# Kernel optimization log

Hardware: AMD Instinct MI355X
Metric: run time of the kernel (lower is better)

Reference implementation:

```python
import jax, jax.numpy as jnp
import numpy as np

B, S, E = 2, 2048, 2048
NQ, NKV, HD = 16, 4, 128
WINDOW = 512
ROPE_BASE = 10000.0


def _rope(x):
    # x: [B, H, S, HD], interleaved even/odd rotation
    half = HD // 2
    freqs = 1.0 / (ROPE_BASE ** (2.0 * jnp.arange(half, dtype=jnp.float32) / HD))
    pos = jnp.arange(x.shape[2], dtype=jnp.float32)
    ang = pos[:, None] * freqs[None, :]            # [S, HD/2]
    cos = jnp.cos(ang)[None, None].astype(x.dtype)  # [1,1,S,HD/2]
    sin = jnp.sin(ang)[None, None].astype(x.dtype)
    xe = x[..., 0::2]
    xo = x[..., 1::2]
    re = xe * cos - xo * sin
    ro = xe * sin + xo * cos
    return jnp.stack([re, ro], axis=-1).reshape(x.shape)


def setup_inputs() -> dict:
    key = jax.random.key(0)
    ks = jax.random.split(key, 9)
    s_in = 1.0 / np.sqrt(E)
    s_out = 1.0 / np.sqrt(NQ * HD)
    return {
        "x": jax.random.normal(ks[0], (B, S, E), jnp.float32),
        "Wq": jax.random.normal(ks[1], (E, NQ * HD), jnp.float32) * s_in,
        "bq": jax.random.normal(ks[2], (NQ * HD,), jnp.float32) * 0.01,
        "Wk": jax.random.normal(ks[3], (E, NKV * HD), jnp.float32) * s_in,
        "bk": jax.random.normal(ks[4], (NKV * HD,), jnp.float32) * 0.01,
        "Wv": jax.random.normal(ks[5], (E, NKV * HD), jnp.float32) * s_in,
        "bv": jax.random.normal(ks[6], (NKV * HD,), jnp.float32) * 0.01,
        "Wo": jax.random.normal(ks[7], (NQ * HD, E), jnp.float32) * s_out,
        "bo": jax.random.normal(ks[8], (E,), jnp.float32) * 0.01,
    }


def reference(x, Wq, bq, Wk, bk, Wv, bv, Wo, bo):
    b, s, _ = x.shape
    q = (x @ Wq + bq).reshape(b, s, NQ, HD).transpose(0, 2, 1, 3)   # [B,NQ,S,HD]
    k = (x @ Wk + bk).reshape(b, s, NKV, HD).transpose(0, 2, 1, 3)  # [B,NKV,S,HD]
    v = (x @ Wv + bv).reshape(b, s, NKV, HD).transpose(0, 2, 1, 3)
    q = _rope(q)
    k = _rope(k)
    rep = NQ // NKV
    k = jnp.repeat(k, rep, axis=1)  # [B,NQ,S,HD], matches torch repeat pattern
    v = jnp.repeat(v, rep, axis=1)
    scores = jnp.einsum("bhqd,bhkd->bhqk", q, k) / np.sqrt(HD)
    i = jnp.arange(s)[:, None]
    j = jnp.arange(s)[None, :]
    allowed = (j <= i) & ((i - j) <= WINDOW)  # sliding-window causal mask
    scores = jnp.where(allowed[None, None], scores, -jnp.inf)
    weights = jax.nn.softmax(scores, axis=-1)
    out = jnp.einsum("bhqk,bhkd->bhqd", weights, v)
    out = out.transpose(0, 2, 1, 3).reshape(b, s, NQ * HD)
    return out @ Wo + bo
```

## Files before the change

### kernel.cpp

```cpp
#include <hip/hip_runtime.h>
#include <hip/hip_bf16.h>
#include <math.h>

#define BB 2
#define SS 2048
#define EE 2048
#define NQ 16
#define NKV 4
#define HD 128
#define WINDOW 512

typedef __hip_bfloat16 bf16;
typedef short short8 __attribute__((ext_vector_type(8)));
typedef float f32x4 __attribute__((ext_vector_type(4)));

__device__ __forceinline__ float toF(bf16 v) { return __bfloat162float(v); }
__device__ __forceinline__ bf16 toB(float v) { return __float2bfloat16(v); }

__device__ __forceinline__ void gld_lds16(const void* g, void* l) {
    __builtin_amdgcn_global_load_lds(
        (const __attribute__((address_space(1))) void*)g,
        (__attribute__((address_space(3))) void*)l, 16, 0, 0);
}

__global__ __launch_bounds__(256) void convert_bf16(const float* __restrict__ in,
                                                    bf16* __restrict__ out, int n) {
    int i = (blockIdx.x * 256 + threadIdx.x) * 4;
    if (i >= n) return;
    const float4 v = *(const float4*)(in + i);
    bf16 o[4] = {toB(v.x), toB(v.y), toB(v.z), toB(v.w)};
    *(uint2*)(out + i) = *(const uint2*)o;
}

__global__ __launch_bounds__(256) void convert_transpose(const float* __restrict__ in,
                                                         bf16* __restrict__ out,
                                                         int K, int N) {
    __shared__ float tile[32][33];
    const int t = threadIdx.x;
    const int tx = t & 31, ty = t >> 5;
    const int n0 = blockIdx.x * 32, k0 = blockIdx.y * 32;
#pragma unroll
    for (int r = 0; r < 4; r++)
        tile[ty + r * 8][tx] = in[(size_t)(k0 + ty + r * 8) * N + n0 + tx];
    __syncthreads();
#pragma unroll
    for (int r = 0; r < 4; r++)
        out[(size_t)(n0 + ty + r * 8) * K + k0 + tx] = toB(tile[tx][ty + r * 8]);
}

__global__ __launch_bounds__(256) void convert_transpose_qkv(
    const float* __restrict__ Wq, const float* __restrict__ Wk,
    const float* __restrict__ Wv, bf16* __restrict__ out) {
    __shared__ float tile[32][33];
    const int t = threadIdx.x;
    const int tx = t & 31, ty = t >> 5;
    const int n0 = blockIdx.x * 32, k0 = blockIdx.y * 32;
    const float* src; int N, nl0;
    if (n0 < 2048)      { src = Wq; N = 2048; nl0 = n0; }
    else if (n0 < 2560) { src = Wk; N = 512;  nl0 = n0 - 2048; }
    else                { src = Wv; N = 512;  nl0 = n0 - 2560; }
#pragma unroll
    for (int r = 0; r < 4; r++)
        tile[ty + r * 8][tx] = src[(size_t)(k0 + ty + r * 8) * N + nl0 + tx];
    __syncthreads();
#pragma unroll
    for (int r = 0; r < 4; r++)
        out[(size_t)(n0 + ty + r * 8) * 2048 + k0 + tx] = toB(tile[tx][ty + r * 8]);
}

template <int MODE>
__global__ __launch_bounds__(256) void mfma_gemm(
    const bf16* __restrict__ A, const bf16* __restrict__ BT,
    const float* __restrict__ b0, const float* __restrict__ b1,
    const float* __restrict__ b2,
    float* __restrict__ Yf,
    bf16* __restrict__ Yq, bf16* __restrict__ Yk, bf16* __restrict__ Yv,
    int M, int N, int K) {
    __shared__ bf16 As[128 * 32];
    __shared__ bf16 Bs[128 * 32];

    const int t = threadIdx.x;
    const int lane = t & 63;
    const int w = t >> 6;
    const int wm = w >> 1, wn = w & 1;
    const int m0 = blockIdx.y * 128, n0 = blockIdx.x * 128;

    const int srow = lane >> 2;
    const int sg   = lane & 3;
    const int scol = (sg ^ ((srow >> 1) & 3)) * 8;

    f32x4 acc[4][4];
#pragma unroll
    for (int i = 0; i < 4; i++)
#pragma unroll
        for (int j = 0; j < 4; j++) acc[i][j] = (f32x4)0.f;

    const int lr = lane & 15;
    const int lq = lane >> 4;
    const int slotr = (lq ^ ((lr >> 1) & 3)) * 8;

    for (int k0 = 0; k0 < K; k0 += 32) {
#pragma unroll
        for (int s = 0; s < 2; s++) {
            const int c = w * 2 + s;
            gld_lds16(A + (size_t)(m0 + c * 16 + srow) * K + k0 + scol, As + c * 512);
            gld_lds16(BT + (size_t)(n0 + c * 16 + srow) * K + k0 + scol, Bs + c * 512);
        }
        __syncthreads();
        short8 af[4], bfv[4];
#pragma unroll
        for (int i = 0; i < 4; i++)
            af[i] = *(const short8*)(As + (wm * 64 + i * 16 + lr) * 32 + slotr);
#pragma unroll
        for (int j = 0; j < 4; j++)
            bfv[j] = *(const short8*)(Bs + (wn * 64 + j * 16 + lr) * 32 + slotr);
#pragma unroll
        for (int i = 0; i < 4; i++)
#pragma unroll
            for (int j = 0; j < 4; j++)
                acc[i][j] = __builtin_amdgcn_mfma_f32_16x16x32_bf16(af[i], bfv[j],
                                                                    acc[i][j], 0, 0, 0);
        __syncthreads();
    }

    if (MODE == 0) {
#pragma unroll
        for (int j = 0; j < 4; j++) {
            const int col = n0 + wn * 64 + j * 16 + lr;
            const float bj = b0[col];
#pragma unroll
            for (int i = 0; i < 4; i++) {
                const int row = m0 + wm * 64 + i * 16 + lq * 4;
#pragma unroll
                for (int r = 0; r < 4; r++)
                    Yf[(size_t)(row + r) * N + col] = acc[i][j][r] + bj;
            }
        }
    } else if (n0 < 2560) {
        bf16* outp; const float* bias; int ldc, c0;
        if (n0 < 2048) { outp = Yq; bias = b0; ldc = 2048; c0 = n0; }
        else           { outp = Yk; bias = b1; ldc = 512;  c0 = n0 - 2048; }
#pragma unroll
        for (int j = 0; j < 4; j++) {
            const int col = c0 + wn * 64 + j * 16 + lr;
            const float bj = bias[col];
            const int d2 = (col & 127) >> 1;
            const bool odd = col & 1;
            const float freq = __expf(-0.14384103622589045f * (float)d2);
#pragma unroll
            for (int i = 0; i < 4; i++) {
                const int row = m0 + wm * 64 + i * 16 + lq * 4;
#pragma unroll
                for (int r = 0; r < 4; r++) {
                    const float v = acc[i][j][r] + bj;
                    const float p = __shfl_xor(v, 1, 64);
                    const float ang = (float)((row + r) & (SS - 1)) * freq;
                    float sn, cs;
                    __sincosf(ang, &sn, &cs);
                    const float o = odd ? (p * sn + v * cs) : (v * cs - p * sn);
                    outp[(size_t)(row + r) * ldc + col] = toB(o);
                }
            }
        }
    } else {
        const int c0 = n0 - 2560;
#pragma unroll
        for (int j = 0; j < 4; j++) {
            const int col = c0 + wn * 64 + j * 16 + lr;
            const float bj = b2[col];
            const int hkv = col >> 7, d = col & 127;
#pragma unroll
            for (int i = 0; i < 4; i++) {
                const int row = m0 + wm * 64 + i * 16 + lq * 4;
                const int bb = row >> 11, sr = row & (SS - 1);
                union { bf16 b[4]; uint2 u; } o4;
#pragma unroll
                for (int r = 0; r < 4; r++) o4.b[r] = toB(acc[i][j][r] + bj);
                *(uint2*)(Yv + (((size_t)bb * NKV + hkv) * HD + d) * SS + sr) = o4.u;
            }
        }
    }
}

__global__ __launch_bounds__(256) void attn_mfma(const bf16* __restrict__ Q,
                                                 const bf16* __restrict__ K,
                                                 const bf16* __restrict__ VT,
                                                 bf16* __restrict__ Oout) {
    __shared__ bf16 Ks[64 * 128];
    __shared__ bf16 Vs[128 * 64];
    __shared__ bf16 Ps[4 * 16 * 72];

    const int t = threadIdx.x;
    const int lane = t & 63;
    const int w = t >> 6;
    const int q0 = blockIdx.x * 64;
    const int h = blockIdx.y;
    const int b = blockIdx.z;
    const int hkv = h >> 2;
    const int lr = lane & 15;
    const int lq = lane >> 4;
    const float scale = 0.08838834764831845f;

    short8 aq[4];
    {
        const int q = q0 + w * 16 + lr;
        const bf16* qp = Q + (((size_t)b * SS + q) * NQ + h) * HD + lq * 8;
#pragma unroll
        for (int ks = 0; ks < 4; ks++) aq[ks] = *(const short8*)(qp + ks * 32);
    }

    const int krow = w * 16 + (lane >> 4);
    const int vrow = w * 32 + (lane >> 3);
    const bf16* Kbase = K + ((size_t)b * SS * NKV + hkv) * HD;
    const bf16* Vbase = VT + (((size_t)b * NKV + hkv) * HD) * SS;

    f32x4 Oa[8];
#pragma unroll
    for (int nb = 0; nb < 8; nb++) Oa[nb] = (f32x4)0.f;
    float mprev[4] = {-3.0e38f, -3.0e38f, -3.0e38f, -3.0e38f};
    float lsum[4] = {0.f, 0.f, 0.f, 0.f};

    bf16* Pw = Ps + w * 16 * 72;
    const int jstart = (q0 >= WINDOW) ? (q0 - WINDOW) : 0;

    for (int c0 = jstart; c0 <= q0; c0 += 64) {
        __syncthreads();
#pragma unroll
        for (int s = 0; s < 4; s++) {
            const int r_ = krow + s * 4;
            const int g_ = (lane & 15) ^ (r_ & 7);
            gld_lds16(Kbase + (size_t)(c0 + r_) * (NKV * HD) + g_ * 8,
                      Ks + (w * 16 + s * 4) * 128);
        }
#pragma unroll
        for (int s = 0; s < 4; s++) {
            const int d_ = vrow + s * 8;
            const int g_ = (lane & 7) ^ (d_ & 7);
            gld_lds16(Vbase + (size_t)d_ * SS + c0 + g_ * 8,
                      Vs + (w * 32 + s * 8) * 64);
        }
        __syncthreads();

        f32x4 sa[4];
#pragma unroll
        for (int nb = 0; nb < 4; nb++) sa[nb] = (f32x4)0.f;
#pragma unroll
        for (int ks = 0; ks < 4; ks++) {
#pragma unroll
            for (int nb = 0; nb < 4; nb++) {
                const int slot = (ks * 4 + lq) ^ (lr & 7);
                short8 bk = *(const short8*)(Ks + (nb * 16 + lr) * 128 + slot * 8);
                sa[nb] = __builtin_amdgcn_mfma_f32_16x16x32_bf16(aq[ks], bk, sa[nb], 0, 0, 0);
            }
        }

        const int rowb = q0 + w * 16 + lq * 4;
        const bool noMask = (c0 + 63 <= q0 + w * 16) &&
                            (q0 + w * 16 + 15 - c0 <= WINDOW);
        float pr[4][4], alpha[4];
#pragma unroll
        for (int r = 0; r < 4; r++) {
            const int row = rowb + r;
            float sv[4];
            float mx = -3.0e38f;
            if (noMask) {
#pragma unroll
                for (int nb = 0; nb < 4; nb++) {
                    const float s = sa[nb][r] * scale;
                    sv[nb] = s;
                    mx = fmaxf(mx, s);
                }
            } else {
#pragma unroll
                for (int nb = 0; nb < 4; nb++) {
                    const int col = c0 + nb * 16 + lr;
                    const bool valid = (col <= row) && (row - col <= WINDOW);
                    const float s = valid ? sa[nb][r] * scale : -3.0e38f;
                    sv[nb] = s;
                    mx = fmaxf(mx, s);
                }
            }
#pragma unroll
            for (int off = 1; off < 16; off <<= 1) mx = fmaxf(mx, __shfl_xor(mx, off, 64));
            const float mn = fmaxf(fmaxf(mprev[r], mx), -1.0e30f);
            alpha[r] = __expf(mprev[r] - mn);
            mprev[r] = mn;
            float rs = 0.f;
#pragma unroll
            for (int nb = 0; nb < 4; nb++) {
                const float p = __expf(sv[nb] - mn);
                pr[r][nb] = p;
                rs += p;
            }
#pragma unroll
            for (int off = 1; off < 16; off <<= 1) rs += __shfl_xor(rs, off, 64);
            lsum[r] = lsum[r] * alpha[r] + rs;
        }

#pragma unroll
        for (int r = 0; r < 4; r++)
#pragma unroll
            for (int nb = 0; nb < 4; nb++)
                Pw[(lq * 4 + r) * 72 + nb * 16 + lr] = toB(pr[r][nb]);

#pragma unroll
        for (int nb = 0; nb < 8; nb++)
#pragma unroll
            for (int r = 0; r < 4; r++) Oa[nb][r] *= alpha[r];
#pragma unroll
        for (int ks = 0; ks < 2; ks++) {
            short8 pa = *(const short8*)(Pw + lr * 72 + ks * 32 + lq * 8);
#pragma unroll
            for (int nb = 0; nb < 8; nb++) {
                const int slot = (ks * 4 + lq) ^ (lr & 7);
                short8 bv = *(const short8*)(Vs + (nb * 16 + lr) * 64 + slot * 8);
                Oa[nb] = __builtin_amdgcn_mfma_f32_16x16x32_bf16(pa, bv, Oa[nb], 0, 0, 0);
            }
        }
    }

    float linv[4];
#pragma unroll
    for (int r = 0; r < 4; r++) linv[r] = 1.f / lsum[r];
    const int rowb = q0 + w * 16 + lq * 4;
#pragma unroll
    for (int nb = 0; nb < 8; nb++)
#pragma unroll
        for (int r = 0; r < 4; r++)
            Oout[(((size_t)b * SS + rowb + r) * NQ + h) * HD + nb * 16 + lr] =
                toB(Oa[nb][r] * linv[r]);
}

extern "C" void kernel_launch(void* const* d_in, const int* in_sizes, int n_in,
                              void* d_out, int out_size, void* d_ws, size_t ws_size,
                              hipStream_t stream) {
    const float* x  = (const float*)d_in[0];
    const float* Wq = (const float*)d_in[1];
    const float* bq = (const float*)d_in[2];
    const float* Wk = (const float*)d_in[3];
    const float* bk = (const float*)d_in[4];
    const float* Wv = (const float*)d_in[5];
    const float* bv = (const float*)d_in[6];
    const float* Wo = (const float*)d_in[7];
    const float* bo = (const float*)d_in[8];
    float* out = (float*)d_out;

    const int M   = BB * SS;
    const int DQ  = NQ * HD;
    const int DKV = NKV * HD;
    const int NPK = DQ + 2 * DKV;

    bf16* xb     = (bf16*)d_ws;
    bf16* WqkvT  = xb + (size_t)M * EE;
    bf16* WoT    = WqkvT + (size_t)NPK * EE;
    bf16* Qb     = WoT + (size_t)EE * DQ;
    bf16* Kb     = Qb + (size_t)M * DQ;
    bf16* Vb     = Kb + (size_t)M * DKV;

    convert_bf16<<<(M * EE / 4 + 255) / 256, 256, 0, stream>>>(x, xb, M * EE);
    convert_transpose_qkv<<<dim3(NPK / 32, EE / 32), 256, 0, stream>>>(Wq, Wk, Wv, WqkvT);
    convert_transpose<<<dim3(DQ / 32, DQ / 32), 256, 0, stream>>>(Wo, WoT, DQ, EE);

    mfma_gemm<1><<<dim3(NPK / 128, M / 128), 256, 0, stream>>>(
        xb, WqkvT, bq, bk, bv, nullptr, Qb, Kb, Vb, M, NPK, EE);

    attn_mfma<<<dim3(SS / 64, NQ, BB), 256, 0, stream>>>(Qb, Kb, Vb, Qb);

    mfma_gemm<0><<<dim3(EE / 128, M / 128), 256, 0, stream>>>(
        Qb, WoT, bo, nullptr, nullptr, out, nullptr, nullptr, nullptr, M, EE, DQ);
}
```

Measured before the change: 333.0 us.

## Use 256x256 double-buffered MFMA GEMM tiles with 512-thread blocks

Replaces the 128x128, K=32 single-buffered GEMM with a 256x256 tile over K=64 steps, run by 8 waves per block. Shared-memory staging is double-buffered: the next K tile is prefetched with global-to-LDS loads while MFMAs run on the current one. It also adds an XOR swizzle for 64-wide rows and raises wave priority around the MFMA bursts. The aim is more data reuse per loaded byte and less exposed load latency. The trade-off is far fewer blocks (192 and 128) than the GPU has CUs, plus 128KB of LDS per block, so only one block fits per CU.

```diff
diff --git a/kernel.cpp b/kernel.cpp
--- a/kernel.cpp
+++ b/kernel.cpp
@@ -69,58 +69,110 @@
 }
 
 template <int MODE>
-__global__ __launch_bounds__(256) void mfma_gemm(
+__global__ __launch_bounds__(512, 2) void mfma_gemm256(
     const bf16* __restrict__ A, const bf16* __restrict__ BT,
     const float* __restrict__ b0, const float* __restrict__ b1,
     const float* __restrict__ b2,
     float* __restrict__ Yf,
     bf16* __restrict__ Yq, bf16* __restrict__ Yk, bf16* __restrict__ Yv,
     int M, int N, int K) {
-    __shared__ bf16 As[128 * 32];
-    __shared__ bf16 Bs[128 * 32];
+    __shared__ __align__(16) bf16 As[2][2][128 * 64];
+    __shared__ __align__(16) bf16 Bs[2][2][128 * 64];
 
     const int t = threadIdx.x;
     const int lane = t & 63;
     const int w = t >> 6;
-    const int wm = w >> 1, wn = w & 1;
-    const int m0 = blockIdx.y * 128, n0 = blockIdx.x * 128;
-
-    const int srow = lane >> 2;
-    const int sg   = lane & 3;
-    const int scol = (sg ^ ((srow >> 1) & 3)) * 8;
-
-    f32x4 acc[4][4];
-#pragma unroll
-    for (int i = 0; i < 4; i++)
-#pragma unroll
-        for (int j = 0; j < 4; j++) acc[i][j] = (f32x4)0.f;
-
+    const int wm = w >> 2;
+    const int wn = w & 3;
+    const int m0 = blockIdx.y * 256, n0 = blockIdx.x * 256;
     const int lr = lane & 15;
     const int lq = lane >> 4;
-    const int slotr = (lq ^ ((lr >> 1) & 3)) * 8;
-
-    for (int k0 = 0; k0 < K; k0 += 32) {
-#pragma unroll
-        for (int s = 0; s < 2; s++) {
-            const int c = w * 2 + s;
-            gld_lds16(A + (size_t)(m0 + c * 16 + srow) * K + k0 + scol, As + c * 512);
-            gld_lds16(BT + (size_t)(n0 + c * 16 + srow) * K + k0 + scol, Bs + c * 512);
-        }
-        __syncthreads();
-        short8 af[4], bfv[4];
-#pragma unroll
-        for (int i = 0; i < 4; i++)
-            af[i] = *(const short8*)(As + (wm * 64 + i * 16 + lr) * 32 + slotr);
-#pragma unroll
-        for (int j = 0; j < 4; j++)
-            bfv[j] = *(const short8*)(Bs + (wn * 64 + j * 16 + lr) * 32 + slotr);
-#pragma unroll
-        for (int i = 0; i < 4; i++)
-#pragma unroll
-            for (int j = 0; j < 4; j++)
-                acc[i][j] = __builtin_amdgcn_mfma_f32_16x16x32_bf16(af[i], bfv[j],
-                                                                    acc[i][j], 0, 0, 0);
-        __syncthreads();
+
+    const int srow8 = lane >> 3;
+    const int sslot = lane & 7;
+    const int NT = K >> 6;
+
+    auto stA = [&](int bi, int h, int kt) {
+#pragma unroll
+        for (int l = 0; l < 2; l++) {
+            const int c = w * 2 + l;
+            const int r = c * 8 + srow8;
+            const int g = sslot ^ (r & 7);
+            gld_lds16(A + (size_t)(m0 + h * 128 + r) * K + kt * 64 + g * 8,
+                      &As[bi][h][c * 512]);
+        }
+    };
+    auto stB = [&](int bi, int h, int kt) {
+#pragma unroll
+        for (int l = 0; l < 2; l++) {
+            const int c = w * 2 + l;
+            const int r = c * 8 + srow8;
+            const int g = sslot ^ (r & 7);
+            gld_lds16(BT + (size_t)(n0 + h * 128 + r) * K + kt * 64 + g * 8,
+                      &Bs[bi][h][c * 512]);
+        }
+    };
+
+    f32x4 acc[8][4];
+#pragma unroll
+    for (int i = 0; i < 8; i++)
+#pragma unroll
+        for (int j = 0; j < 4; j++) acc[i][j] = (f32x4)0.f;
+
+    stA(0, 0, 0); stA(0, 1, 0); stB(0, 0, 0); stB(0, 1, 0);
+    asm volatile("s_waitcnt vmcnt(0)" ::: "memory");
+    __builtin_amdgcn_s_barrier();
+
+    const int brh0 = (wn & 1) * 64;
+    const int bh = wn >> 1;
+
+    for (int kt = 0; kt < NT; kt++) {
+        const int bi = kt & 1;
+        const bool pf = (kt + 1 < NT);
+        const bf16* Aw = &As[bi][wm][0];
+        const bf16* Bw = &Bs[bi][bh][0];
+        short8 bfr[4][2];
+#pragma unroll
+        for (int p = 0; p < 4; p++) {
+            if (p == 0 && pf) { stA(bi ^ 1, 0, kt + 1); stA(bi ^ 1, 1, kt + 1); }
+            if (p == 1 && pf) { stB(bi ^ 1, 0, kt + 1); stB(bi ^ 1, 1, kt + 1); }
+            if (p == 0) {
+#pragma unroll
+                for (int j = 0; j < 4; j++)
+#pragma unroll
+                    for (int kk = 0; kk < 2; kk++) {
+                        const int rh = brh0 + j * 16 + lr;
+                        const int slot = ((kk << 2) + lq) ^ (lr & 7);
+                        bfr[j][kk] = *(const short8*)(Bw + rh * 64 + slot * 8);
+                    }
+            }
+            short8 afr[2][2];
+#pragma unroll
+            for (int i2 = 0; i2 < 2; i2++)
+#pragma unroll
+                for (int kk = 0; kk < 2; kk++) {
+                    const int rh = (p * 2 + i2) * 16 + lr;
+                    const int slot = ((kk << 2) + lq) ^ (lr & 7);
+                    afr[i2][kk] = *(const short8*)(Aw + rh * 64 + slot * 8);
+                }
+            __builtin_amdgcn_s_barrier();
+            __builtin_amdgcn_s_setprio(1);
+#pragma unroll
+            for (int i2 = 0; i2 < 2; i2++)
+#pragma unroll
+                for (int j = 0; j < 4; j++)
+#pragma unroll
+                    for (int kk = 0; kk < 2; kk++)
+                        acc[p * 2 + i2][j] = __builtin_amdgcn_mfma_f32_16x16x32_bf16(
+                            afr[i2][kk], bfr[j][kk], acc[p * 2 + i2][j], 0, 0, 0);
+            __builtin_amdgcn_s_setprio(0);
+            if (p < 3) {
+                __builtin_amdgcn_s_barrier();
+            } else {
+                asm volatile("s_waitcnt vmcnt(0)" ::: "memory");
+                __builtin_amdgcn_s_barrier();
+            }
+        }
     }
 
     if (MODE == 0) {
@@ -129,8 +181,8 @@
             const int col = n0 + wn * 64 + j * 16 + lr;
             const float bj = b0[col];
 #pragma unroll
-            for (int i = 0; i < 4; i++) {
-                const int row = m0 + wm * 64 + i * 16 + lq * 4;
+            for (int i = 0; i < 8; i++) {
+                const int row = m0 + wm * 128 + i * 16 + lq * 4;
 #pragma unroll
                 for (int r = 0; r < 4; r++)
                     Yf[(size_t)(row + r) * N + col] = acc[i][j][r] + bj;
@@ -148,8 +200,8 @@
             const bool odd = col & 1;
             const float freq = __expf(-0.14384103622589045f * (float)d2);
 #pragma unroll
-            for (int i = 0; i < 4; i++) {
-                const int row = m0 + wm * 64 + i * 16 + lq * 4;
+            for (int i = 0; i < 8; i++) {
+                const int row = m0 + wm * 128 + i * 16 + lq * 4;
 #pragma unroll
                 for (int r = 0; r < 4; r++) {
                     const float v = acc[i][j][r] + bj;
@@ -170,8 +222,8 @@
             const float bj = b2[col];
             const int hkv = col >> 7, d = col & 127;
 #pragma unroll
-            for (int i = 0; i < 4; i++) {
-                const int row = m0 + wm * 64 + i * 16 + lq * 4;
+            for (int i = 0; i < 8; i++) {
+                const int row = m0 + wm * 128 + i * 16 + lq * 4;
                 const int bb = row >> 11, sr = row & (SS - 1);
                 union { bf16 b[4]; uint2 u; } o4;
 #pragma unroll
@@ -361,11 +413,11 @@
     convert_transpose_qkv<<<dim3(NPK / 32, EE / 32), 256, 0, stream>>>(Wq, Wk, Wv, WqkvT);
     convert_transpose<<<dim3(DQ / 32, DQ / 32), 256, 0, stream>>>(Wo, WoT, DQ, EE);
 
-    mfma_gemm<1><<<dim3(NPK / 128, M / 128), 256, 0, stream>>>(
+    mfma_gemm256<1><<<dim3(NPK / 256, M / 256), 512, 0, stream>>>(
         xb, WqkvT, bq, bk, bv, nullptr, Qb, Kb, Vb, M, NPK, EE);
 
     attn_mfma<<<dim3(SS / 64, NQ, BB), 256, 0, stream>>>(Qb, Kb, Vb, Qb);
 
-    mfma_gemm<0><<<dim3(EE / 128, M / 128), 256, 0, stream>>>(
+    mfma_gemm256<0><<<dim3(EE / 256, M / 256), 512, 0, stream>>>(
         Qb, WoT, bo, nullptr, nullptr, out, nullptr, nullptr, nullptr, M, EE, DQ);
 }
```

New measurement: 360.8 us. 8.4% more time.

## Rewrite projection GEMMs with larger tiles, 512 threads and double-buffered LDS prefetch

Applied to the files above, without the earlier changes.

Replaces the 128x128, 4-warp GEMM with a templated 8-warp kernel using 256x256 tiles for the QKV projection and 256x128 tiles for the output projection. Each tile is a K-step of 64 split into two 32-wide halves, and the halves are prefetched into double-buffered LDS using explicit vmcnt waits and raw barriers. MFMA bursts are raised in wave priority, aiming to overlap global loads with math and get more reuse per tile. The trade-offs are fewer blocks for the QKV GEMM (under one wave on the device) and a dropped LDS XOR swizzle, which may bring back bank conflicts on fragment reads.

```diff
diff --git a/kernel.cpp b/kernel.cpp
--- a/kernel.cpp
+++ b/kernel.cpp
@@ -21,6 +21,14 @@
     __builtin_amdgcn_global_load_lds(
         (const __attribute__((address_space(1))) void*)g,
         (__attribute__((address_space(3))) void*)l, 16, 0, 0);
+}
+
+template <int V> __device__ __forceinline__ void waitvm() {
+    if constexpr (V == 8)      asm volatile("s_waitcnt vmcnt(8)" ::: "memory");
+    else if constexpr (V == 6) asm volatile("s_waitcnt vmcnt(6)" ::: "memory");
+    else if constexpr (V == 4) asm volatile("s_waitcnt vmcnt(4)" ::: "memory");
+    else if constexpr (V == 3) asm volatile("s_waitcnt vmcnt(3)" ::: "memory");
+    else                       asm volatile("s_waitcnt vmcnt(0)" ::: "memory");
 }
 
 __global__ __launch_bounds__(256) void convert_bf16(const float* __restrict__ in,
@@ -68,69 +76,106 @@
         out[(size_t)(n0 + ty + r * 8) * 2048 + k0 + tx] = toB(tile[tx][ty + r * 8]);
 }
 
-template <int MODE>
-__global__ __launch_bounds__(256) void mfma_gemm(
+template <int MODE, int BM, int BN, int WARPS_M>
+__global__ __launch_bounds__(512, 2) void mfma_gemm_v3(
     const bf16* __restrict__ A, const bf16* __restrict__ BT,
     const float* __restrict__ b0, const float* __restrict__ b1,
     const float* __restrict__ b2,
     float* __restrict__ Yf,
     bf16* __restrict__ Yq, bf16* __restrict__ Yk, bf16* __restrict__ Yv,
     int M, int N, int K) {
-    __shared__ bf16 As[128 * 32];
-    __shared__ bf16 Bs[128 * 32];
+    constexpr int WARPS_N = 8 / WARPS_M;
+    constexpr int NI = BM / WARPS_M / 16;
+    constexpr int NJ = BN / WARPS_N / 16;
+    constexpr int LA = BM / 128;
+    constexpr int LB = BN / 128;
+    constexpr int PL = LA + LB;
+
+    __shared__ __align__(16) bf16 As[2][2][BM * 32];
+    __shared__ __align__(16) bf16 Bs[2][2][BN * 32];
 
     const int t = threadIdx.x;
     const int lane = t & 63;
     const int w = t >> 6;
-    const int wm = w >> 1, wn = w & 1;
-    const int m0 = blockIdx.y * 128, n0 = blockIdx.x * 128;
-
-    const int srow = lane >> 2;
-    const int sg   = lane & 3;
-    const int scol = (sg ^ ((srow >> 1) & 3)) * 8;
-
-    f32x4 acc[4][4];
-#pragma unroll
-    for (int i = 0; i < 4; i++)
-#pragma unroll
-        for (int j = 0; j < 4; j++) acc[i][j] = (f32x4)0.f;
-
+    const int wm = w / WARPS_N;
+    const int wn = w % WARPS_N;
+    const int m0 = blockIdx.y * BM, n0 = blockIdx.x * BN;
     const int lr = lane & 15;
     const int lq = lane >> 4;
-    const int slotr = (lq ^ ((lr >> 1) & 3)) * 8;
-
-    for (int k0 = 0; k0 < K; k0 += 32) {
-#pragma unroll
-        for (int s = 0; s < 2; s++) {
-            const int c = w * 2 + s;
-            gld_lds16(A + (size_t)(m0 + c * 16 + srow) * K + k0 + scol, As + c * 512);
-            gld_lds16(BT + (size_t)(n0 + c * 16 + srow) * K + k0 + scol, Bs + c * 512);
-        }
-        __syncthreads();
-        short8 af[4], bfv[4];
-#pragma unroll
-        for (int i = 0; i < 4; i++)
-            af[i] = *(const short8*)(As + (wm * 64 + i * 16 + lr) * 32 + slotr);
-#pragma unroll
-        for (int j = 0; j < 4; j++)
-            bfv[j] = *(const short8*)(Bs + (wn * 64 + j * 16 + lr) * 32 + slotr);
-#pragma unroll
-        for (int i = 0; i < 4; i++)
-#pragma unroll
-            for (int j = 0; j < 4; j++)
+    const int NT = K >> 6;
+
+    auto stA = [&](int bi, int kk, int kt) {
+#pragma unroll
+        for (int l = 0; l < LA; l++) {
+            const int c = w * LA + l;
+            gld_lds16(A + (size_t)(m0 + c * 16 + (lane >> 2)) * K +
+                          kt * 64 + kk * 32 + (lane & 3) * 8,
+                      &As[bi][kk][c * 512]);
+        }
+    };
+    auto stB = [&](int bi, int kk, int kt) {
+#pragma unroll
+        for (int l = 0; l < LB; l++) {
+            const int c = w * LB + l;
+            gld_lds16(BT + (size_t)(n0 + c * 16 + (lane >> 2)) * K +
+                           kt * 64 + kk * 32 + (lane & 3) * 8,
+                      &Bs[bi][kk][c * 512]);
+        }
+    };
+
+    f32x4 acc[NI][NJ];
+#pragma unroll
+    for (int i = 0; i < NI; i++)
+#pragma unroll
+        for (int j = 0; j < NJ; j++) acc[i][j] = (f32x4)0.f;
+
+    auto phase = [&](int bi, int kk) {
+        const bf16* Aslc = &As[bi][kk][0];
+        const bf16* Bslc = &Bs[bi][kk][0];
+        short8 af[NI], bfv[NJ];
+#pragma unroll
+        for (int i = 0; i < NI; i++)
+            af[i] = *(const short8*)(Aslc + (wm * (NI * 16) + i * 16 + lr) * 32 + lq * 8);
+#pragma unroll
+        for (int j = 0; j < NJ; j++)
+            bfv[j] = *(const short8*)(Bslc + (wn * (NJ * 16) + j * 16 + lr) * 32 + lq * 8);
+        __builtin_amdgcn_s_setprio(1);
+#pragma unroll
+        for (int i = 0; i < NI; i++)
+#pragma unroll
+            for (int j = 0; j < NJ; j++)
                 acc[i][j] = __builtin_amdgcn_mfma_f32_16x16x32_bf16(af[i], bfv[j],
                                                                     acc[i][j], 0, 0, 0);
-        __syncthreads();
+        __builtin_amdgcn_s_setprio(0);
+    };
+
+    stA(0, 0, 0); stB(0, 0, 0);
+    stA(0, 1, 0); stB(0, 1, 0);
+
+    for (int kt = 0; kt < NT; kt++) {
+        const int bi = kt & 1;
+        const bool pf = (kt + 1 < NT);
+        if (pf) { stA(bi ^ 1, 0, kt + 1); stB(bi ^ 1, 0, kt + 1); waitvm<2 * PL>(); }
+        else    { waitvm<PL>(); }
+        __builtin_amdgcn_s_barrier();
+        __builtin_amdgcn_sched_barrier(0);
+        phase(bi, 0);
+        if (pf) { stA(bi ^ 1, 1, kt + 1); stB(bi ^ 1, 1, kt + 1); waitvm<2 * PL>(); }
+        else    { waitvm<0>(); }
+        __builtin_amdgcn_s_barrier();
+        __builtin_amdgcn_sched_barrier(0);
+        phase(bi, 1);
+        __builtin_amdgcn_s_barrier();
     }
 
     if (MODE == 0) {
 #pragma unroll
-        for (int j = 0; j < 4; j++) {
-            const int col = n0 + wn * 64 + j * 16 + lr;
+        for (int j = 0; j < NJ; j++) {
+            const int col = n0 + wn * (NJ * 16) + j * 16 + lr;
             const float bj = b0[col];
 #pragma unroll
-            for (int i = 0; i < 4; i++) {
-                const int row = m0 + wm * 64 + i * 16 + lq * 4;
+            for (int i = 0; i < NI; i++) {
+                const int row = m0 + wm * (NI * 16) + i * 16 + lq * 4;
 #pragma unroll
                 for (int r = 0; r < 4; r++)
                     Yf[(size_t)(row + r) * N + col] = acc[i][j][r] + bj;
@@ -141,15 +186,15 @@
         if (n0 < 2048) { outp = Yq; bias = b0; ldc = 2048; c0 = n0; }
         else           { outp = Yk; bias = b1; ldc = 512;  c0 = n0 - 2048; }
 #pragma unroll
-        for (int j = 0; j < 4; j++) {
-            const int col = c0 + wn * 64 + j * 16 + lr;
+        for (int j = 0; j < NJ; j++) {
+            const int col = c0 + wn * (NJ * 16) + j * 16 + lr;
             const float bj = bias[col];
             const int d2 = (col & 127) >> 1;
             const bool odd = col & 1;
             const float freq = __expf(-0.14384103622589045f * (float)d2);
 #pragma unroll
-            for (int i = 0; i < 4; i++) {
-                const int row = m0 + wm * 64 + i * 16 + lq * 4;
+            for (int i = 0; i < NI; i++) {
+                const int row = m0 + wm * (NI * 16) + i * 16 + lq * 4;
 #pragma unroll
                 for (int r = 0; r < 4; r++) {
                     const float v = acc[i][j][r] + bj;
@@ -165,13 +210,13 @@
     } else {
         const int c0 = n0 - 2560;
 #pragma unroll
-        for (int j = 0; j < 4; j++) {
-            const int col = c0 + wn * 64 + j * 16 + lr;
+        for (int j = 0; j < NJ; j++) {
+            const int col = c0 + wn * (NJ * 16) + j * 16 + lr;
             const float bj = b2[col];
             const int hkv = col >> 7, d = col & 127;
 #pragma unroll
-            for (int i = 0; i < 4; i++) {
-                const int row = m0 + wm * 64 + i * 16 + lq * 4;
+            for (int i = 0; i < NI; i++) {
+                const int row = m0 + wm * (NI * 16) + i * 16 + lq * 4;
                 const int bb = row >> 11, sr = row & (SS - 1);
                 union { bf16 b[4]; uint2 u; } o4;
 #pragma unroll
@@ -361,11 +406,11 @@
     convert_transpose_qkv<<<dim3(NPK / 32, EE / 32), 256, 0, stream>>>(Wq, Wk, Wv, WqkvT);
     convert_transpose<<<dim3(DQ / 32, DQ / 32), 256, 0, stream>>>(Wo, WoT, DQ, EE);
 
-    mfma_gemm<1><<<dim3(NPK / 128, M / 128), 256, 0, stream>>>(
+    mfma_gemm_v3<1, 256, 256, 2><<<dim3(NPK / 256, M / 256), 512, 0, stream>>>(
         xb, WqkvT, bq, bk, bv, nullptr, Qb, Kb, Vb, M, NPK, EE);
 
     attn_mfma<<<dim3(SS / 64, NQ, BB), 256, 0, stream>>>(Qb, Kb, Vb, Qb);
 
-    mfma_gemm<0><<<dim3(EE / 128, M / 128), 256, 0, stream>>>(
+    mfma_gemm_v3<0, 256, 128, 4><<<dim3(EE / 128, M / 256), 512, 0, stream>>>(
         Qb, WoT, bo, nullptr, nullptr, out, nullptr, nullptr, nullptr, M, EE, DQ);
 }
```

Result: no change. 327.5 us (-1.7%).
